# Optimization experiments

Measured on AMD Instinct MI355X. Metric: run time of the kernel, lower is better.

Reference implementation:

```python
import jax, jax.numpy as jnp
import numpy as np

CHUNK = 64


def _rmsnorm(x, g, eps=1e-6):
    return x * jax.lax.rsqrt(jnp.mean(x * x, axis=-1, keepdims=True) + eps) * g


def setup_inputs() -> dict:
    key = jax.random.key(0)
    ks = jax.random.split(key, 8)
    B, L, D, N = 4, 4096, 512, 64
    s = 0.02
    return {
        'x': jax.random.normal(ks[0], (B, L, D), jnp.float32),
        'A_log': -jnp.ones((D,), jnp.float32) * jnp.log(2.0),
        'dt_bias': jnp.log(jnp.expm1(jax.random.uniform(ks[1], (D,), jnp.float32, 0.001, 0.1))),
        'D_skip': jnp.ones((D,), jnp.float32),
        'W_xproj': jax.random.normal(ks[2], (D, 2 * D), jnp.float32) * s,
        'b_xproj': jnp.zeros((2 * D,), jnp.float32),
        'W_B': jax.random.normal(ks[3], (D, N), jnp.float32) * s,
        'W_C': jax.random.normal(ks[4], (D, N), jnp.float32) * s,
        'W_dt': jax.random.normal(ks[5], (D, D), jnp.float32) * s,
        'g_Bnorm': jnp.ones((N,), jnp.float32),
        'g_Cnorm': jnp.ones((N,), jnp.float32),
        'g_outnorm': jnp.ones((D,), jnp.float32),
        'W_out': jax.random.normal(ks[6], (D, D), jnp.float32) * s,
        'b_out': jnp.zeros((D,), jnp.float32),
    }


def reference(x, A_log, dt_bias, D_skip, W_xproj, b_xproj, W_B, W_C, W_dt,
              g_Bnorm, g_Cnorm, g_outnorm, W_out, b_out):
    b, l, d = x.shape
    n = W_B.shape[1]
    p = CHUNK
    c = l // p  # L chosen divisible by chunk size (original pads otherwise)

    A = -jnp.exp(jnp.clip(A_log, -20.0, 2.0))  # (d,)
    xp = x @ W_xproj + b_xproj                  # (b,l,2d)
    x_bar, z = jnp.split(xp, 2, axis=-1)
    Bm = _rmsnorm(x_bar @ W_B, g_Bnorm)         # (b,l,n)
    Cm = _rmsnorm(x_bar @ W_C, g_Cnorm)         # (b,l,n)
    dt = jnp.clip(jax.nn.softplus(x_bar @ W_dt + dt_bias), 1e-4, 5.0)
    A_bar = jnp.exp(jnp.clip(dt * A, -20.0, 0.0))  # (b,l,d)

    to_chunks = lambda t: t.reshape(b, c, p, t.shape[-1]).transpose(1, 0, 2, 3)
    xc, Bc, Cc, Ac = map(to_chunks, (x_bar, Bm, Cm, A_bar))  # (c,b,p,*)
    mask = jnp.tril(jnp.ones((p, p), x.dtype))

    def process_chunk(prev_state, inputs):
        x_c, B_c, C_c, A_c = inputs
        log_a = jnp.log(jnp.clip(A_c, 1e-8, 1.0))
        la_cs = jnp.cumsum(log_a, axis=1)  # (b,p,d)
        # intra-chunk decay matrix M: (b,p,p,d)
        M = jnp.exp(la_cs[:, :, None, :] - la_cs[:, None, :, :]) * mask[None, :, :, None]
        BX = jnp.einsum('bpn,bpd->bpnd', B_c, x_c)
        state = jnp.einsum('bijd,bjnd->bind', M, BX)
        y_intra = jnp.einsum('bpn,bpnd->bpd', C_c, state)
        decay = jnp.exp(la_cs)
        y_inter = jnp.einsum('bpn,bpnd->bpd', C_c,
                             prev_state[:, None, :, :] * decay[:, :, None, :])
        y_c = y_intra + y_inter
        a_total = jnp.exp(la_cs[:, -1, :])             # (b,d)
        a_to_end = jnp.exp(la_cs[:, -1:, :] - la_cs)   # (b,p,d)
        chunk_state = jnp.einsum('bpn,bpd->bnd', B_c, x_c * a_to_end)
        new_state = prev_state * a_total[:, None, :] + chunk_state
        new_state = jnp.where(jnp.isfinite(new_state), new_state, 0.0)
        y_c = jnp.where(jnp.isfinite(y_c), y_c, 0.0)
        return new_state, y_c

    init = jnp.zeros((b, n, d), x.dtype)
    _, yc = jax.lax.scan(jax.checkpoint(process_chunk), init, (xc, Bc, Cc, Ac))
    y = yc.transpose(1, 0, 2, 3).reshape(b, l, d)
    y = jnp.where(jnp.isfinite(y), y, 0.0)
    y = y + D_skip * x_bar
    y = _rmsnorm(y, g_outnorm) * jax.nn.silu(z)
    return y @ W_out + b_out
```

## Files before the change

kernel.cpp:

```cpp
#include <hip/hip_runtime.h>
#include <hip/hip_bf16.h>
#include <math.h>

typedef __hip_bfloat16 bf16;
typedef __attribute__((ext_vector_type(8))) short short8;
typedef __attribute__((ext_vector_type(4))) float floatx4;
typedef __attribute__((ext_vector_type(2))) float floatx2;

#define B_ 4
#define L_ 4096
#define D_ 512
#define M_ (B_*L_)

__device__ __forceinline__ float b2f(bf16 v){ return __bfloat162float(v); }
__device__ __forceinline__ bf16  f2b(float v){ return __float2bfloat16(v); }
__device__ __forceinline__ short f2bs(float v){ bf16 h = __float2bfloat16(v); short s; __builtin_memcpy(&s,&h,2); return s; }
__device__ __forceinline__ unsigned short f2bus(float v){ bf16 h = __float2bfloat16(v); unsigned short s; __builtin_memcpy(&s,&h,2); return s; }
__device__ __forceinline__ float bus2f(unsigned short u){ unsigned int x = ((unsigned int)u)<<16; float f; __builtin_memcpy(&f,&x,4); return f; }
__device__ __forceinline__ floatx2 fx2(float v){ floatx2 r; r.x=v; r.y=v; return r; }

#define GLD16(gp, lp) __builtin_amdgcn_global_load_lds( \
    (const __attribute__((address_space(1))) void*)(gp), \
    (__attribute__((address_space(3))) void*)(lp), 16, 0, 0)

__global__ __launch_bounds__(1024) void k_transpose(const float* __restrict__ src,
                                                    bf16* __restrict__ dst, int K, int N){
    __shared__ float tile[32][33];
    int n0 = blockIdx.x*32, k0 = blockIdx.y*32;
    int tx = threadIdx.x, ty = threadIdx.y;
    tile[ty][tx] = src[(size_t)(k0+ty)*N + n0+tx];
    __syncthreads();
    ((short*)dst)[(size_t)(n0+ty)*K + k0+tx] = f2bs(tile[tx][ty]);
}

__global__ __launch_bounds__(256) void k_cvt(const float* __restrict__ src,
                                             bf16* __restrict__ dst){
    size_t i = ((size_t)blockIdx.x*256 + threadIdx.x)*4;
    float4 v = *(const float4*)(src + i);
    short4 s; s.x=f2bs(v.x); s.y=f2bs(v.y); s.z=f2bs(v.z); s.w=f2bs(v.w);
    *(short4*)((short*)dst + i) = s;
}

template<int EPI>
__global__ __launch_bounds__(256) void k_gemm(const bf16* __restrict__ Ap,
        const bf16* __restrict__ Wt, const float* __restrict__ bias,
        const float* __restrict__ aux,
        float* __restrict__ o1, bf16* __restrict__ o2, bf16* __restrict__ o3,
        float* __restrict__ o4){
    __shared__ short As[128*32];
    __shared__ short Bs[128*32];
    const int K = 512;
    int m0 = blockIdx.x*128, n0 = blockIdx.y*128;
    int tid=threadIdx.x, w=tid>>6, lane=tid&63;
    int wr=w>>1, wc=w&1, quad=lane>>4, r16=lane&15;
    floatx4 acc[4][4];
    #pragma unroll
    for (int i=0;i<4;i++)
        #pragma unroll
        for (int j=0;j<4;j++)
            #pragma unroll
            for (int e=0;e<4;e++) acc[i][j][e]=0.f;

    int c0 = tid, c1 = tid + 256;
    const short* Ab = (const short*)Ap + (size_t)m0*K;
    const short* Wb = (const short*)Wt + (size_t)n0*K;
    int r0 = c0>>2, g0 = (c0&3)*8;
    int r1 = c1>>2, g1 = (c1&3)*8;

    for (int k0=0;k0<K;k0+=32){
        GLD16(Ab + (size_t)r0*K + k0 + g0, &As[c0*8]);
        GLD16(Ab + (size_t)r1*K + k0 + g1, &As[c1*8]);
        GLD16(Wb + (size_t)r0*K + k0 + g0, &Bs[c0*8]);
        GLD16(Wb + (size_t)r1*K + k0 + g1, &Bs[c1*8]);
        __syncthreads();
        short8 af[4], bv[4];
        #pragma unroll
        for (int i=0;i<4;i++) af[i] = *(short8*)&As[(wr*64+i*16+r16)*32 + quad*8];
        #pragma unroll
        for (int j=0;j<4;j++) bv[j] = *(short8*)&Bs[(wc*64+j*16+r16)*32 + quad*8];
        #pragma unroll
        for (int i=0;i<4;i++)
            #pragma unroll
            for (int j=0;j<4;j++)
                acc[i][j] = __builtin_amdgcn_mfma_f32_16x16x32_bf16(af[i], bv[j], acc[i][j], 0,0,0);
        __syncthreads();
    }
    if (EPI==3){
        #pragma unroll
        for (int i=0;i<4;i++)
        #pragma unroll
        for (int reg=0;reg<4;reg++){
            float ss=0.f;
            #pragma unroll
            for (int j=0;j<4;j++){ float t=acc[i][j][reg]; ss+=t*t; }
            #pragma unroll
            for (int m=1;m<16;m<<=1) ss += __shfl_xor(ss, m, 64);
            float rq = rsqrtf(ss*(1.f/64.f)+1e-6f);
            int gr = m0 + wr*64 + i*16 + quad*4 + reg;
            #pragma unroll
            for (int j=0;j<4;j++){
                int gc = wc*64 + j*16 + r16;
                float gval = (gc<64) ? bias[gc] : aux[gc-64];
                float v = acc[i][j][reg]*rq*gval;
                if (gc<64) o1[(size_t)gr*64 + gc] = v;
                else       o4[(size_t)gr*64 + (gc-64)] = v;
            }
        }
        return;
    }
    #pragma unroll
    for (int i=0;i<4;i++)
    #pragma unroll
    for (int j=0;j<4;j++)
    #pragma unroll
    for (int reg=0;reg<4;reg++){
        int gr = m0 + wr*64 + i*16 + quad*4 + reg;
        int gc = n0 + wc*64 + j*16 + r16;
        float v = acc[i][j][reg] + bias[gc];
        if (EPI==0){
            if (gc < 512){
                o1[(size_t)gr*512 + gc] = v;
                o2[(size_t)gr*512 + gc] = f2b(v);
            } else {
                o3[(size_t)gr*512 + (gc-512)] = f2b(v / (1.f + __expf(-v)));
            }
        } else if (EPI==1){
            float sp = (v > 15.f) ? v : log1pf(__expf(v));
            float dt = fminf(fmaxf(sp, 1e-4f), 5.f);
            float Ad = -__expf(fminf(fmaxf(aux[gc], -20.f), 2.f));
            o1[(size_t)gr*512 + gc] = fminf(fmaxf(dt*Ad, -18.420680743952367f), 0.f);
        } else {
            o1[(size_t)gr*512 + gc] = v;
        }
    }
}

__global__ __launch_bounds__(256) void k_pass1(const float* __restrict__ la,
        const float* __restrict__ xbar, const float* __restrict__ Bm,
        unsigned short* __restrict__ localh, float* __restrict__ atot){
    __shared__ float Bs[64*32];
    int c=blockIdx.x, b=blockIdx.y, nh=blockIdx.z;
    int d = threadIdx.x*2;
    size_t rowbase=(size_t)b*L_+(size_t)c*64;
    size_t cb=(size_t)c*4+b;
    #pragma unroll
    for (int it=0;it<2;it++){
        int idx=it*256+threadIdx.x;
        int row=idx>>3, grp=idx&7;
        *(float4*)&Bs[row*32+grp*4] = *(const float4*)(Bm + (rowbase+row)*64 + nh*32 + grp*4);
    }
    __syncthreads();
    floatx2 st[32];
    #pragma unroll
    for (int n=0;n<32;n++) st[n]=fx2(0.f);
    floatx2 cs=fx2(0.f);
    size_t off0=rowbase*512+d;
    floatx2 la_n=*(const floatx2*)(la+off0), x_n=*(const floatx2*)(xbar+off0);
    #pragma unroll 2
    for (int i=0;i<64;i++){
        floatx2 lai=la_n, xi=x_n;
        if (i<63){ la_n=*(const floatx2*)(la+off0+(i+1)*512);
                   x_n =*(const floatx2*)(xbar+off0+(i+1)*512); }
        floatx2 ai; ai.x=__expf(lai.x); ai.y=__expf(lai.y);
        cs = cs + lai;
        const float* Br=Bs+i*32;
        #pragma unroll
        for (int k=0;k<8;k++){
            float4 bv=*(const float4*)(Br+k*4);
            st[k*4+0]=ai*st[k*4+0]+fx2(bv.x)*xi;
            st[k*4+1]=ai*st[k*4+1]+fx2(bv.y)*xi;
            st[k*4+2]=ai*st[k*4+2]+fx2(bv.z)*xi;
            st[k*4+3]=ai*st[k*4+3]+fx2(bv.w)*xi;
        }
    }
    #pragma unroll
    for (int n=0;n<32;n++){
        ushort2 p; p.x=f2bus(st[n].x); p.y=f2bus(st[n].y);
        *(ushort2*)(localh + (cb*64 + nh*32 + n)*512 + d) = p;
    }
    if (nh==0){
        floatx2 at; at.x=__expf(cs.x); at.y=__expf(cs.y);
        *(floatx2*)(atot + cb*512 + d) = at;
    }
}

__global__ __launch_bounds__(256) void k_scan(unsigned short* __restrict__ localh,
        const float* __restrict__ atot){
    int idx = blockIdx.x*256 + threadIdx.x;
    int d = (idx & 255)*2, n = (idx >> 8) & 63, b = idx >> 14;
    float sx=0.f, sy=0.f;
    for (int c=0;c<64;c++){
        size_t cb = (size_t)c*4 + b;
        size_t off = (cb*64 + n)*512 + d;
        ushort2 v = *(ushort2*)(localh+off);
        float vx=bus2f(v.x), vy=bus2f(v.y);
        ushort2 wp; wp.x=f2bus(sx); wp.y=f2bus(sy);
        *(ushort2*)(localh+off) = wp;
        float2 at = *(const float2*)(atot + cb*512 + d);
        sx = sx*at.x + vx; sy = sy*at.y + vy;
        if (!isfinite(sx)) sx = 0.f;
        if (!isfinite(sy)) sy = 0.f;
    }
}

__global__ __launch_bounds__(256) void k_pass2(const float* __restrict__ la,
        const float* __restrict__ xbar, const float* __restrict__ Bm,
        const float* __restrict__ Cm, const unsigned short* __restrict__ Sprevh,
        float* __restrict__ ybuf){
    __shared__ float Bs[64*32];
    __shared__ float Cs[64*32];
    int c=blockIdx.x, b=blockIdx.y, nh=blockIdx.z;
    int d = threadIdx.x*2;
    size_t rowbase=(size_t)b*L_+(size_t)c*64;
    size_t cb=(size_t)c*4+b;
    #pragma unroll
    for (int it=0;it<2;it++){
        int idx=it*256+threadIdx.x;
        int row=idx>>3, grp=idx&7;
        *(float4*)&Bs[row*32+grp*4] = *(const float4*)(Bm + (rowbase+row)*64 + nh*32 + grp*4);
        *(float4*)&Cs[row*32+grp*4] = *(const float4*)(Cm + (rowbase+row)*64 + nh*32 + grp*4);
    }
    floatx2 st[32];
    #pragma unroll
    for (int n=0;n<32;n++){
        ushort2 p = *(const ushort2*)(Sprevh + (cb*64 + nh*32 + n)*512 + d);
        st[n].x = bus2f(p.x); st[n].y = bus2f(p.y);
    }
    __syncthreads();
    size_t off0=rowbase*512+d;
    float* yout = ybuf + (size_t)nh*M_*512;
    floatx2 la_n=*(const floatx2*)(la+off0), x_n=*(const floatx2*)(xbar+off0);
    #pragma unroll 2
    for (int i=0;i<64;i++){
        floatx2 lai=la_n, xi=x_n;
        if (i<63){ la_n=*(const floatx2*)(la+off0+(i+1)*512);
                   x_n =*(const floatx2*)(xbar+off0+(i+1)*512); }
        floatx2 ai; ai.x=__expf(lai.x); ai.y=__expf(lai.y);
        const float* Br=Bs+i*32;
        const float* Cr=Cs+i*32;
        floatx2 yv=fx2(0.f);
        #pragma unroll
        for (int k=0;k<8;k++){
            float4 bv=*(const float4*)(Br+k*4);
            float4 cv=*(const float4*)(Cr+k*4);
            floatx2 s;
            s=ai*st[k*4+0]+fx2(bv.x)*xi; st[k*4+0]=s; yv=yv+fx2(cv.x)*s;
            s=ai*st[k*4+1]+fx2(bv.y)*xi; st[k*4+1]=s; yv=yv+fx2(cv.y)*s;
            s=ai*st[k*4+2]+fx2(bv.z)*xi; st[k*4+2]=s; yv=yv+fx2(cv.z)*s;
            s=ai*st[k*4+3]+fx2(bv.w)*xi; st[k*4+3]=s; yv=yv+fx2(cv.w)*s;
        }
        *(floatx2*)(yout + off0 + (size_t)i*512) = yv;
    }
}

__global__ __launch_bounds__(256) void k_outnorm(const float* __restrict__ yA,
        const float* __restrict__ yB,
        const float* __restrict__ xbar, const float* __restrict__ Dskip,
        const float* __restrict__ g, const bf16* __restrict__ siluz,
        bf16* __restrict__ u){
    int wave = threadIdx.x >> 6, lane = threadIdx.x & 63;
    size_t row = (size_t)blockIdx.x*4 + wave;
    float v[8]; float ss = 0.f;
    #pragma unroll
    for (int j=0;j<8;j++){
        int d = j*64 + lane;
        float yv = yA[row*512 + d] + yB[row*512 + d];
        if (!isfinite(yv)) yv = 0.f;
        float t = yv + Dskip[d] * xbar[row*512 + d];
        v[j] = t; ss += t*t;
    }
    #pragma unroll
    for (int m=1;m<64;m<<=1) ss += __shfl_xor(ss, m, 64);
    float r = rsqrtf(ss*(1.f/512.f) + 1e-6f);
    #pragma unroll
    for (int j=0;j<8;j++){
        int d = j*64 + lane;
        u[row*512 + d] = f2b(v[j] * r * g[d] * b2f(siluz[row*512 + d]));
    }
}

extern "C" void kernel_launch(void* const* d_in, const int* in_sizes, int n_in,
                              void* d_out, int out_size, void* d_ws, size_t ws_size,
                              hipStream_t stream){
    const float* x       = (const float*)d_in[0];
    const float* A_log   = (const float*)d_in[1];
    const float* dt_bias = (const float*)d_in[2];
    const float* D_skip  = (const float*)d_in[3];
    const float* W_xproj = (const float*)d_in[4];
    const float* b_xproj = (const float*)d_in[5];
    const float* W_B     = (const float*)d_in[6];
    const float* W_C     = (const float*)d_in[7];
    const float* W_dt    = (const float*)d_in[8];
    const float* g_B     = (const float*)d_in[9];
    const float* g_C     = (const float*)d_in[10];
    const float* g_out   = (const float*)d_in[11];
    const float* W_out   = (const float*)d_in[12];
    const float* b_out   = (const float*)d_in[13];
    float* out = (float*)d_out;

    char* wp = (char*)d_ws;
    auto alloc = [&](size_t bytes)->char*{ char* p = wp; wp += (bytes + 255) & ~(size_t)255; return p; };
    float* xbar  = (float*)alloc((size_t)M_*512*4);
    bf16*  xh    = (bf16*) alloc((size_t)M_*512*2);
    bf16*  xbarh = (bf16*) alloc((size_t)M_*512*2);
    bf16*  siluz = (bf16*) alloc((size_t)M_*512*2);
    float* la    = (float*)alloc((size_t)M_*512*4);
    float* Bm    = (float*)alloc((size_t)M_*64*4);
    float* Cm    = (float*)alloc((size_t)M_*64*4);
    unsigned short* localh = (unsigned short*)alloc((size_t)256*64*512*2);
    float* atot  = (float*)alloc((size_t)256*512*4);
    float* ybuf  = (float*)alloc((size_t)2*M_*512*4);
    bf16*  u     = (bf16*) alloc((size_t)M_*512*2);
    bf16*  WtX   = (bf16*) alloc((size_t)1024*512*2);
    bf16*  WtD   = (bf16*) alloc((size_t)512*512*2);
    bf16*  WtO   = (bf16*) alloc((size_t)512*512*2);
    bf16*  WtBC  = (bf16*) alloc((size_t)128*512*2);

    dim3 tb(32,32);
    k_transpose<<<dim3(32,16), tb, 0, stream>>>(W_xproj, WtX, 512, 1024);
    k_transpose<<<dim3(16,16), tb, 0, stream>>>(W_dt,   WtD, 512, 512);
    k_transpose<<<dim3(16,16), tb, 0, stream>>>(W_out,  WtO, 512, 512);
    k_transpose<<<dim3(2,16),  tb, 0, stream>>>(W_B,    WtBC,          512, 64);
    k_transpose<<<dim3(2,16),  tb, 0, stream>>>(W_C,    WtBC+64*512,   512, 64);
    k_cvt      <<<M_*512/1024, 256, 0, stream>>>(x, xh);

    k_gemm<0> <<<dim3(128, 8), 256, 0, stream>>>(xh,    WtX,  b_xproj, nullptr, xbar, xbarh, siluz, nullptr);
    k_gemm<3> <<<dim3(128, 1), 256, 0, stream>>>(xbarh, WtBC, g_B, g_C, Bm, nullptr, nullptr, Cm);
    k_gemm<1> <<<dim3(128, 4), 256, 0, stream>>>(xbarh, WtD,  dt_bias, A_log, la, nullptr, nullptr, nullptr);
    k_pass1   <<<dim3(64,4,2), 256, 0, stream>>>(la, xbar, Bm, localh, atot);
    k_scan    <<<256,          256, 0, stream>>>(localh, atot);
    k_pass2   <<<dim3(64,4,2), 256, 0, stream>>>(la, xbar, Bm, Cm, localh, ybuf);
    k_outnorm <<<M_/4,         256, 0, stream>>>(ybuf, ybuf+(size_t)M_*512, xbar, D_skip, g_out, siluz, u);
    k_gemm<2> <<<dim3(128, 4), 256, 0, stream>>>(u,     WtO,  b_out, nullptr, out, nullptr, nullptr, nullptr);
}
```

Before: 355.1 us.

## Store scan intermediates in bf16 and widen per-thread work in scan passes

Drops the fp32 copies of x_bar and log-decay and keeps only bf16 versions, which the chunked scan passes and the output-norm kernel now read. The per-head partial outputs from pass2 are also written in bf16, roughly halving the traffic through the memory-bound intermediate buffers. Pass1 and pass2 now give each thread 4 channels with 128-thread blocks and drop the manual prefetch and unrolling, so each thread holds more state registers and there are fewer waves. This lowers precision of the decay and activations, which could affect accuracy through the recurrence.

After: 382.1 us. +7.6%, slower.

```diff
diff --git a/kernel.cpp b/kernel.cpp
--- a/kernel.cpp
+++ b/kernel.cpp
@@ -5,7 +5,6 @@
 typedef __hip_bfloat16 bf16;
 typedef __attribute__((ext_vector_type(8))) short short8;
 typedef __attribute__((ext_vector_type(4))) float floatx4;
-typedef __attribute__((ext_vector_type(2))) float floatx2;
 
 #define B_ 4
 #define L_ 4096
@@ -17,7 +16,10 @@
 __device__ __forceinline__ short f2bs(float v){ bf16 h = __float2bfloat16(v); short s; __builtin_memcpy(&s,&h,2); return s; }
 __device__ __forceinline__ unsigned short f2bus(float v){ bf16 h = __float2bfloat16(v); unsigned short s; __builtin_memcpy(&s,&h,2); return s; }
 __device__ __forceinline__ float bus2f(unsigned short u){ unsigned int x = ((unsigned int)u)<<16; float f; __builtin_memcpy(&f,&x,4); return f; }
-__device__ __forceinline__ floatx2 fx2(float v){ floatx2 r; r.x=v; r.y=v; return r; }
+__device__ __forceinline__ floatx4 fx4(float v){ floatx4 r; r.x=v; r.y=v; r.z=v; r.w=v; return r; }
+__device__ __forceinline__ floatx4 us4f(ushort4 u){ floatx4 r; r.x=bus2f(u.x); r.y=bus2f(u.y); r.z=bus2f(u.z); r.w=bus2f(u.w); return r; }
+__device__ __forceinline__ ushort4 f4us(floatx4 v){ ushort4 r; r.x=f2bus(v.x); r.y=f2bus(v.y); r.z=f2bus(v.z); r.w=f2bus(v.w); return r; }
+__device__ __forceinline__ floatx4 exp4(floatx4 v){ floatx4 r; r.x=__expf(v.x); r.y=__expf(v.y); r.z=__expf(v.z); r.w=__expf(v.w); return r; }
 
 #define GLD16(gp, lp) __builtin_amdgcn_global_load_lds( \
     (const __attribute__((address_space(1))) void*)(gp), \
@@ -119,7 +121,6 @@
         float v = acc[i][j][reg] + bias[gc];
         if (EPI==0){
             if (gc < 512){
-                o1[(size_t)gr*512 + gc] = v;
                 o2[(size_t)gr*512 + gc] = f2b(v);
             } else {
                 o3[(size_t)gr*512 + (gc-512)] = f2b(v / (1.f + __expf(-v)));
@@ -128,59 +129,55 @@
             float sp = (v > 15.f) ? v : log1pf(__expf(v));
             float dt = fminf(fmaxf(sp, 1e-4f), 5.f);
             float Ad = -__expf(fminf(fmaxf(aux[gc], -20.f), 2.f));
-            o1[(size_t)gr*512 + gc] = fminf(fmaxf(dt*Ad, -18.420680743952367f), 0.f);
+            o2[(size_t)gr*512 + gc] = f2b(fminf(fmaxf(dt*Ad, -18.420680743952367f), 0.f));
         } else {
             o1[(size_t)gr*512 + gc] = v;
         }
     }
 }
 
-__global__ __launch_bounds__(256) void k_pass1(const float* __restrict__ la,
-        const float* __restrict__ xbar, const float* __restrict__ Bm,
+__global__ __launch_bounds__(128) void k_pass1(const unsigned short* __restrict__ lah,
+        const unsigned short* __restrict__ xh, const float* __restrict__ Bm,
         unsigned short* __restrict__ localh, float* __restrict__ atot){
     __shared__ float Bs[64*32];
     int c=blockIdx.x, b=blockIdx.y, nh=blockIdx.z;
-    int d = threadIdx.x*2;
+    int d = threadIdx.x*4;
     size_t rowbase=(size_t)b*L_+(size_t)c*64;
     size_t cb=(size_t)c*4+b;
     #pragma unroll
-    for (int it=0;it<2;it++){
-        int idx=it*256+threadIdx.x;
+    for (int it=0;it<4;it++){
+        int idx=it*128+threadIdx.x;
         int row=idx>>3, grp=idx&7;
         *(float4*)&Bs[row*32+grp*4] = *(const float4*)(Bm + (rowbase+row)*64 + nh*32 + grp*4);
     }
     __syncthreads();
-    floatx2 st[32];
-    #pragma unroll
-    for (int n=0;n<32;n++) st[n]=fx2(0.f);
-    floatx2 cs=fx2(0.f);
+    floatx4 st[32];
+    #pragma unroll
+    for (int n=0;n<32;n++) st[n]=fx4(0.f);
+    floatx4 cs=fx4(0.f);
     size_t off0=rowbase*512+d;
-    floatx2 la_n=*(const floatx2*)(la+off0), x_n=*(const floatx2*)(xbar+off0);
-    #pragma unroll 2
+    #pragma unroll 1
     for (int i=0;i<64;i++){
-        floatx2 lai=la_n, xi=x_n;
-        if (i<63){ la_n=*(const floatx2*)(la+off0+(i+1)*512);
-                   x_n =*(const floatx2*)(xbar+off0+(i+1)*512); }
-        floatx2 ai; ai.x=__expf(lai.x); ai.y=__expf(lai.y);
+        floatx4 lai = us4f(*(const ushort4*)(lah+off0+(size_t)i*512));
+        floatx4 xi  = us4f(*(const ushort4*)(xh +off0+(size_t)i*512));
+        floatx4 ai = exp4(lai);
         cs = cs + lai;
         const float* Br=Bs+i*32;
         #pragma unroll
         for (int k=0;k<8;k++){
             float4 bv=*(const float4*)(Br+k*4);
-            st[k*4+0]=ai*st[k*4+0]+fx2(bv.x)*xi;
-            st[k*4+1]=ai*st[k*4+1]+fx2(bv.y)*xi;
-            st[k*4+2]=ai*st[k*4+2]+fx2(bv.z)*xi;
-            st[k*4+3]=ai*st[k*4+3]+fx2(bv.w)*xi;
+            st[k*4+0]=ai*st[k*4+0]+fx4(bv.x)*xi;
+            st[k*4+1]=ai*st[k*4+1]+fx4(bv.y)*xi;
+            st[k*4+2]=ai*st[k*4+2]+fx4(bv.z)*xi;
+            st[k*4+3]=ai*st[k*4+3]+fx4(bv.w)*xi;
         }
     }
     #pragma unroll
-    for (int n=0;n<32;n++){
-        ushort2 p; p.x=f2bus(st[n].x); p.y=f2bus(st[n].y);
-        *(ushort2*)(localh + (cb*64 + nh*32 + n)*512 + d) = p;
-    }
+    for (int n=0;n<32;n++)
+        *(ushort4*)(localh + (cb*64 + nh*32 + n)*512 + d) = f4us(st[n]);
     if (nh==0){
-        floatx2 at; at.x=__expf(cs.x); at.y=__expf(cs.y);
-        *(floatx2*)(atot + cb*512 + d) = at;
+        floatx4 at = exp4(cs);
+        *(floatx4*)(atot + cb*512 + d) = at;
     }
 }
 
@@ -203,59 +200,55 @@
     }
 }
 
-__global__ __launch_bounds__(256) void k_pass2(const float* __restrict__ la,
-        const float* __restrict__ xbar, const float* __restrict__ Bm,
+__global__ __launch_bounds__(128) void k_pass2(const unsigned short* __restrict__ lah,
+        const unsigned short* __restrict__ xh, const float* __restrict__ Bm,
         const float* __restrict__ Cm, const unsigned short* __restrict__ Sprevh,
-        float* __restrict__ ybuf){
+        unsigned short* __restrict__ ybuf){
     __shared__ float Bs[64*32];
     __shared__ float Cs[64*32];
     int c=blockIdx.x, b=blockIdx.y, nh=blockIdx.z;
-    int d = threadIdx.x*2;
+    int d = threadIdx.x*4;
     size_t rowbase=(size_t)b*L_+(size_t)c*64;
     size_t cb=(size_t)c*4+b;
     #pragma unroll
-    for (int it=0;it<2;it++){
-        int idx=it*256+threadIdx.x;
+    for (int it=0;it<4;it++){
+        int idx=it*128+threadIdx.x;
         int row=idx>>3, grp=idx&7;
         *(float4*)&Bs[row*32+grp*4] = *(const float4*)(Bm + (rowbase+row)*64 + nh*32 + grp*4);
         *(float4*)&Cs[row*32+grp*4] = *(const float4*)(Cm + (rowbase+row)*64 + nh*32 + grp*4);
     }
-    floatx2 st[32];
-    #pragma unroll
-    for (int n=0;n<32;n++){
-        ushort2 p = *(const ushort2*)(Sprevh + (cb*64 + nh*32 + n)*512 + d);
-        st[n].x = bus2f(p.x); st[n].y = bus2f(p.y);
-    }
+    floatx4 st[32];
+    #pragma unroll
+    for (int n=0;n<32;n++)
+        st[n] = us4f(*(const ushort4*)(Sprevh + (cb*64 + nh*32 + n)*512 + d));
     __syncthreads();
     size_t off0=rowbase*512+d;
-    float* yout = ybuf + (size_t)nh*M_*512;
-    floatx2 la_n=*(const floatx2*)(la+off0), x_n=*(const floatx2*)(xbar+off0);
-    #pragma unroll 2
+    unsigned short* yout = ybuf + (size_t)nh*M_*512;
+    #pragma unroll 1
     for (int i=0;i<64;i++){
-        floatx2 lai=la_n, xi=x_n;
-        if (i<63){ la_n=*(const floatx2*)(la+off0+(i+1)*512);
-                   x_n =*(const floatx2*)(xbar+off0+(i+1)*512); }
-        floatx2 ai; ai.x=__expf(lai.x); ai.y=__expf(lai.y);
+        floatx4 lai = us4f(*(const ushort4*)(lah+off0+(size_t)i*512));
+        floatx4 xi  = us4f(*(const ushort4*)(xh +off0+(size_t)i*512));
+        floatx4 ai = exp4(lai);
         const float* Br=Bs+i*32;
         const float* Cr=Cs+i*32;
-        floatx2 yv=fx2(0.f);
+        floatx4 yv=fx4(0.f);
         #pragma unroll
         for (int k=0;k<8;k++){
             float4 bv=*(const float4*)(Br+k*4);
             float4 cv=*(const float4*)(Cr+k*4);
-            floatx2 s;
-            s=ai*st[k*4+0]+fx2(bv.x)*xi; st[k*4+0]=s; yv=yv+fx2(cv.x)*s;
-            s=ai*st[k*4+1]+fx2(bv.y)*xi; st[k*4+1]=s; yv=yv+fx2(cv.y)*s;
-            s=ai*st[k*4+2]+fx2(bv.z)*xi; st[k*4+2]=s; yv=yv+fx2(cv.z)*s;
-            s=ai*st[k*4+3]+fx2(bv.w)*xi; st[k*4+3]=s; yv=yv+fx2(cv.w)*s;
+            floatx4 s;
+            s=ai*st[k*4+0]+fx4(bv.x)*xi; st[k*4+0]=s; yv=yv+fx4(cv.x)*s;
+            s=ai*st[k*4+1]+fx4(bv.y)*xi; st[k*4+1]=s; yv=yv+fx4(cv.y)*s;
+            s=ai*st[k*4+2]+fx4(bv.z)*xi; st[k*4+2]=s; yv=yv+fx4(cv.z)*s;
+            s=ai*st[k*4+3]+fx4(bv.w)*xi; st[k*4+3]=s; yv=yv+fx4(cv.w)*s;
         }
-        *(floatx2*)(yout + off0 + (size_t)i*512) = yv;
-    }
-}
-
-__global__ __launch_bounds__(256) void k_outnorm(const float* __restrict__ yA,
-        const float* __restrict__ yB,
-        const float* __restrict__ xbar, const float* __restrict__ Dskip,
+        *(ushort4*)(yout + off0 + (size_t)i*512) = f4us(yv);
+    }
+}
+
+__global__ __launch_bounds__(256) void k_outnorm(const unsigned short* __restrict__ yA,
+        const unsigned short* __restrict__ yB,
+        const bf16* __restrict__ xbarh, const float* __restrict__ Dskip,
         const float* __restrict__ g, const bf16* __restrict__ siluz,
         bf16* __restrict__ u){
     int wave = threadIdx.x >> 6, lane = threadIdx.x & 63;
@@ -264,9 +257,9 @@
     #pragma unroll
     for (int j=0;j<8;j++){
         int d = j*64 + lane;
-        float yv = yA[row*512 + d] + yB[row*512 + d];
+        float yv = bus2f(yA[row*512 + d]) + bus2f(yB[row*512 + d]);
         if (!isfinite(yv)) yv = 0.f;
-        float t = yv + Dskip[d] * xbar[row*512 + d];
+        float t = yv + Dskip[d] * b2f(xbarh[row*512 + d]);
         v[j] = t; ss += t*t;
     }
     #pragma unroll
@@ -300,16 +293,15 @@
 
     char* wp = (char*)d_ws;
     auto alloc = [&](size_t bytes)->char*{ char* p = wp; wp += (bytes + 255) & ~(size_t)255; return p; };
-    float* xbar  = (float*)alloc((size_t)M_*512*4);
     bf16*  xh    = (bf16*) alloc((size_t)M_*512*2);
     bf16*  xbarh = (bf16*) alloc((size_t)M_*512*2);
     bf16*  siluz = (bf16*) alloc((size_t)M_*512*2);
-    float* la    = (float*)alloc((size_t)M_*512*4);
+    bf16*  lah   = (bf16*) alloc((size_t)M_*512*2);
     float* Bm    = (float*)alloc((size_t)M_*64*4);
     float* Cm    = (float*)alloc((size_t)M_*64*4);
     unsigned short* localh = (unsigned short*)alloc((size_t)256*64*512*2);
     float* atot  = (float*)alloc((size_t)256*512*4);
-    float* ybuf  = (float*)alloc((size_t)2*M_*512*4);
+    unsigned short* ybuf = (unsigned short*)alloc((size_t)2*M_*512*2);
     bf16*  u     = (bf16*) alloc((size_t)M_*512*2);
     bf16*  WtX   = (bf16*) alloc((size_t)1024*512*2);
     bf16*  WtD   = (bf16*) alloc((size_t)512*512*2);
@@ -324,12 +316,12 @@
     k_transpose<<<dim3(2,16),  tb, 0, stream>>>(W_C,    WtBC+64*512,   512, 64);
     k_cvt      <<<M_*512/1024, 256, 0, stream>>>(x, xh);
 
-    k_gemm<0> <<<dim3(128, 8), 256, 0, stream>>>(xh,    WtX,  b_xproj, nullptr, xbar, xbarh, siluz, nullptr);
+    k_gemm<0> <<<dim3(128, 8), 256, 0, stream>>>(xh,    WtX,  b_xproj, nullptr, nullptr, xbarh, siluz, nullptr);
     k_gemm<3> <<<dim3(128, 1), 256, 0, stream>>>(xbarh, WtBC, g_B, g_C, Bm, nullptr, nullptr, Cm);
-    k_gemm<1> <<<dim3(128, 4), 256, 0, stream>>>(xbarh, WtD,  dt_bias, A_log, la, nullptr, nullptr, nullptr);
-    k_pass1   <<<dim3(64,4,2), 256, 0, stream>>>(la, xbar, Bm, localh, atot);
+    k_gemm<1> <<<dim3(128, 4), 256, 0, stream>>>(xbarh, WtD,  dt_bias, A_log, nullptr, lah, nullptr, nullptr);
+    k_pass1   <<<dim3(64,4,2), 128, 0, stream>>>((const unsigned short*)lah, (const unsigned short*)xbarh, Bm, localh, atot);
     k_scan    <<<256,          256, 0, stream>>>(localh, atot);
-    k_pass2   <<<dim3(64,4,2), 256, 0, stream>>>(la, xbar, Bm, Cm, localh, ybuf);
-    k_outnorm <<<M_/4,         256, 0, stream>>>(ybuf, ybuf+(size_t)M_*512, xbar, D_skip, g_out, siluz, u);
+    k_pass2   <<<dim3(64,4,2), 128, 0, stream>>>((const unsigned short*)lah, (const unsigned short*)xbarh, Bm, Cm, localh, ybuf);
+    k_outnorm <<<M_/4,         256, 0, stream>>>(ybuf, ybuf+(size_t)M_*512, xbarh, D_skip, g_out, siluz, u);
     k_gemm<2> <<<dim3(128, 4), 256, 0, stream>>>(u,     WtO,  b_out, nullptr, out, nullptr, nullptr, nullptr);
 }
```
